# Performance work log

Measured on AMD Instinct MI355X. Metric: run time of the kernel, lower is better.

Reference implementation:

```python
import jax, jax.numpy as jnp
import numpy as np

B, S, D = 1, 2048, 2048
H, G = 32, 8            # n_heads, n_groups
HPG = H // G            # heads per group = 4
HD = D // H             # head_dim = 64


def setup_inputs() -> dict:
    key = jax.random.key(0)
    ks = jax.random.split(key, 5)
    w_scale = 0.02
    return {
        "x":  jax.random.normal(ks[0], (B, S, D), dtype=jnp.float32),
        "Wq": jax.random.normal(ks[1], (D, D), dtype=jnp.float32) * w_scale,
        "bq": jnp.zeros((D,), dtype=jnp.float32),
        "Wk": jax.random.normal(ks[2], (G * HD, D), dtype=jnp.float32) * w_scale,
        "bk": jnp.zeros((G * HD,), dtype=jnp.float32),
        "Wv": jax.random.normal(ks[3], (G * HD, D), dtype=jnp.float32) * w_scale,
        "bv": jnp.zeros((G * HD,), dtype=jnp.float32),
        "Wo": jax.random.normal(ks[4], (D, D), dtype=jnp.float32) * w_scale,
        "bo": jnp.zeros((D,), dtype=jnp.float32),
    }


def reference(x, Wq, bq, Wk, bk, Wv, bv, Wo, bo):
    b, n, _ = x.shape
    # projections (torch Linear: y = x @ W.T + b)
    q = x @ Wq.T + bq                              # [b, n, D]
    k = x @ Wk.T + bk                              # [b, n, G*HD]
    v = x @ Wv.T + bv                              # [b, n, G*HD]
    # q: [b, n, H, HD] -> [b, H, n, HD] -> split heads as (g h): [b, G, HPG, n, HD]
    q = q.reshape(b, n, H, HD).transpose(0, 2, 1, 3).reshape(b, G, HPG, n, HD)
    k = k.reshape(b, n, G, HD).transpose(0, 2, 1, 3)   # [b, G, n, HD]
    v = v.reshape(b, n, G, HD).transpose(0, 2, 1, 3)   # [b, G, n, HD]
    scale = 1.0 / jnp.sqrt(jnp.asarray(HD, dtype=q.dtype))
    attn_score = jnp.einsum('bghnd,bgsd->bghns', q, k) * scale
    attn_prob = jax.nn.softmax(attn_score, axis=-1)
    out = jnp.einsum('bghns,bgsd->bghnd', attn_prob, v)   # [b, G, HPG, n, HD]
    # faithful to original: rearrange 'b g h n d -> b n (h g d)' (h-major, g-minor)
    out = out.transpose(0, 3, 2, 1, 4).reshape(b, n, HPG * G * HD)
    return out @ Wo.T + bo
```

## Files before the change

### kernel.cpp

```cpp
#include <hip/hip_runtime.h>
#include <hip/hip_bf16.h>

constexpr int kS   = 2048;
constexpr int kD   = 2048;
constexpr int kG   = 8;
constexpr int kHD  = 64;
constexpr int kGHD = 512;
constexpr int kNQKV = kD + 2 * kGHD;

constexpr float kQScale = 0.125f * 1.4426950408889634f;

typedef __attribute__((ext_vector_type(8)))  _Float16 f16x8;
typedef __attribute__((ext_vector_type(4)))  float    f32x4;
typedef __attribute__((ext_vector_type(16))) float    f32x16;
typedef __attribute__((ext_vector_type(4)))  unsigned int u32x4;

__device__ __forceinline__ ushort f2h(float x) {
    return __builtin_bit_cast(ushort, (_Float16)x);
}
__device__ __forceinline__ float fast_exp2(float x) {
    return __builtin_amdgcn_exp2f(x);
}
__device__ __forceinline__ unsigned int pkrtz(float a, float b) {
    auto r = __builtin_amdgcn_cvt_pkrtz(a, b);
    return __builtin_bit_cast(unsigned int, r);
}

__global__ __launch_bounds__(256) void cvt_f16(
    const float* __restrict__ in, ushort* __restrict__ out, int n, float scale)
{
    const int i = (blockIdx.x * 256 + threadIdx.x) * 4;
    if (i >= n) return;
    const float4 x = *(const float4*)&in[i];
    ushort4 o;
    o.x = f2h(x.x * scale); o.y = f2h(x.y * scale);
    o.z = f2h(x.z * scale); o.w = f2h(x.w * scale);
    *(ushort4*)&out[i] = o;
}

__global__ __launch_bounds__(256) void prep_bias(
    const float* __restrict__ bq, const float* __restrict__ bk,
    const float* __restrict__ bv, float* __restrict__ bqkv)
{
    const int i = blockIdx.x * 256 + threadIdx.x;
    if (i < kD)             bqkv[i] = bq[i] * kQScale;
    else if (i < kD + kGHD) bqkv[i] = bk[i - kD];
    else if (i < kNQKV)     bqkv[i] = bv[i - kD - kGHD];
}

__device__ __forceinline__ int xcd_swizzle(int orig, int nwg) {
    const int cpx = nwg >> 3;
    return (orig & 7) * cpx + (orig >> 3);
}

#define GEMM_PRELUDE(Aptr, Bptr)                                              \
    const int bid  = xcd_swizzle(blockIdx.x, gridDim.x);                      \
    const int m0   = (bid / gridX) * 128;                                     \
    const int n0   = (bid % gridX) * 128;                                     \
    const int tid  = threadIdx.x;                                             \
    const int w    = tid >> 6;                                                \
    const int lane = tid & 63;                                                \
    const int wm   = w >> 2;                                                  \
    const int wn   = w & 3;                                                   \
    const int fr   = lane & 15;                                               \
    const int kq   = lane >> 4;                                               \
    const int srow = w * 16 + (lane >> 2);                                    \
    const int sslot = ((lane & 3) ^ ((lane >> 3) & 3)) * 8;                   \
    const ushort* gA = (Aptr) + (size_t)(m0 + srow) * K + sslot;              \
    const ushort* gB = (Bptr) + (size_t)(n0 + srow) * K + sslot;              \
    const int pslot = (kq ^ ((fr >> 1) & 3)) * 8;                             \
    f32x4 acc[4][2];                                                          \
    _Pragma("unroll")                                                         \
    for (int mi = 0; mi < 4; ++mi)                                            \
        _Pragma("unroll")                                                     \
        for (int ni = 0; ni < 2; ++ni) {                                      \
            f32x4 z = {0.f, 0.f, 0.f, 0.f};                                   \
            acc[mi][ni] = z;                                                  \
        }

#define GEMM_STAGE(buf, k0)                                                   \
    do {                                                                      \
        __builtin_amdgcn_global_load_lds(                                     \
            (const __attribute__((address_space(1))) void*)(gA + (k0)),       \
            (__attribute__((address_space(3))) void*)&lds[buf][0][w * 512],   \
            16, 0, 0);                                                        \
        __builtin_amdgcn_global_load_lds(                                     \
            (const __attribute__((address_space(1))) void*)(gB + (k0)),       \
            (__attribute__((address_space(3))) void*)&lds[buf][1][w * 512],   \
            16, 0, 0);                                                        \
    } while (0)

#define GEMM_KLOOP(MFMA_BODY)                                                 \
    GEMM_STAGE(0, 0);                                                         \
    __syncthreads();                                                          \
    int cur = 0;                                                              \
    for (int k0 = 0; k0 < K; k0 += 32) {                                      \
        if (k0 + 32 < K) GEMM_STAGE(cur ^ 1, k0 + 32);                        \
        f16x8 af[4], bf[2];                                                   \
        _Pragma("unroll")                                                     \
        for (int f = 0; f < 4; ++f)                                           \
            af[f] = *(const f16x8*)&lds[cur][0][(wm * 64 + f * 16 + fr) * 32 + pslot]; \
        _Pragma("unroll")                                                     \
        for (int f = 0; f < 2; ++f)                                           \
            bf[f] = *(const f16x8*)&lds[cur][1][(wn * 32 + f * 16 + fr) * 32 + pslot]; \
        __builtin_amdgcn_s_setprio(1);                                        \
        MFMA_BODY                                                             \
        __builtin_amdgcn_s_setprio(0);                                        \
        __syncthreads();                                                      \
        cur ^= 1;                                                             \
    }

__global__ __launch_bounds__(512) void gemm_qkv(
    const ushort* __restrict__ Af, const ushort* __restrict__ Bf,
    const float* __restrict__ bias,
    ushort* __restrict__ qb16, ushort* __restrict__ kb16, ushort* __restrict__ vt16,
    int K, int gridX)
{
    __shared__ ushort lds[2][2][128 * 32];

    GEMM_PRELUDE(Af, Bf)
    GEMM_KLOOP(
        _Pragma("unroll")
        for (int mi = 0; mi < 4; ++mi)
            _Pragma("unroll")
            for (int ni = 0; ni < 2; ++ni)
                acc[mi][ni] = __builtin_amdgcn_mfma_f32_16x16x32_f16(
                    af[mi], bf[ni], acc[mi][ni], 0, 0, 0);
    )

    const int seg = (n0 < kD) ? 0 : (n0 < kD + kGHD) ? 1 : 2;
    #pragma unroll
    for (int ni = 0; ni < 2; ++ni) {
        const int ncol = n0 + wn * 32 + ni * 16 + fr;
        const float bv = bias[ncol];
        #pragma unroll
        for (int mi = 0; mi < 4; ++mi) {
            #pragma unroll
            for (int i = 0; i < 4; ++i) {
                const int row = m0 + wm * 64 + mi * 16 + kq * 4 + i;
                const ushort u = f2h(acc[mi][ni][i] + bv);
                if (seg == 0)      qb16[(size_t)row * kD   + ncol]              = u;
                else if (seg == 1) kb16[(size_t)row * kGHD + (ncol - kD)]       = u;
                else               vt16[(size_t)(ncol - kD - kGHD) * kS + row]  = u;
            }
        }
    }
}

__global__ __launch_bounds__(512) void gemm_o(
    const ushort* __restrict__ Af, const ushort* __restrict__ Bf,
    const float* __restrict__ bias, float* __restrict__ C, int K, int N, int gridX)
{
    __shared__ ushort lds[2][2][128 * 32];

    GEMM_PRELUDE(Af, Bf)
    GEMM_KLOOP(
        _Pragma("unroll")
        for (int mi = 0; mi < 4; ++mi)
            _Pragma("unroll")
            for (int ni = 0; ni < 2; ++ni)
                acc[mi][ni] = __builtin_amdgcn_mfma_f32_16x16x32_f16(
                    af[mi], bf[ni], acc[mi][ni], 0, 0, 0);
    )

    #pragma unroll
    for (int ni = 0; ni < 2; ++ni) {
        const int ncol = n0 + wn * 32 + ni * 16 + fr;
        const float bv = bias[ncol];
        #pragma unroll
        for (int mi = 0; mi < 4; ++mi)
            #pragma unroll
            for (int i = 0; i < 4; ++i) {
                const int row = m0 + wm * 64 + mi * 16 + kq * 4 + i;
                C[(size_t)row * N + ncol] = acc[mi][ni][i] + bv;
            }
    }
}

__global__ __launch_bounds__(512) void gqa_attn_mfma(
    const ushort* __restrict__ qb,
    const ushort* __restrict__ kb,
    const ushort* __restrict__ vt,
    ushort* __restrict__ oh)
{
    __shared__ ushort Kt[2][2][64 * 64];
    __shared__ ushort Vt[2][2][64 * 64];

    const int g    = blockIdx.y;
    const int q0   = blockIdx.x * 32;
    const int tid  = threadIdx.x;
    const int w    = tid >> 6;
    const int lane = tid & 63;
    const int hw   = w & 3;
    const int half = w >> 2;
    const int ql   = lane & 31;
    const int hi   = lane >> 5;
    const int h    = g * 4 + hw;
    const int tbase = half * (kS / 2);

    const int r0 = hw * 16 + (lane >> 3);
    const int ss = (lane & 7) ^ (r0 & 7);

#define ATTN_STAGE(buf, t)                                                         \
    do {                                                                           \
        __builtin_amdgcn_global_load_lds(                                          \
            (const __attribute__((address_space(1))) void*)                       \
                (kb + (size_t)(tbase + (t) + r0) * kGHD + g * kHD + ss * 8),       \
            (__attribute__((address_space(3))) void*)(&Kt[half][buf][(hw * 16) * 64]), \
            16, 0, 0);                                                             \
        __builtin_amdgcn_global_load_lds(                                          \
            (const __attribute__((address_space(1))) void*)                       \
                (kb + (size_t)(tbase + (t) + r0 + 8) * kGHD + g * kHD + ss * 8),   \
            (__attribute__((address_space(3))) void*)(&Kt[half][buf][(hw * 16 + 8) * 64]), \
            16, 0, 0);                                                             \
        __builtin_amdgcn_global_load_lds(                                          \
            (const __attribute__((address_space(1))) void*)                       \
                (vt + (size_t)(g * kHD + r0) * kS + tbase + (t) + ss * 8),         \
            (__attribute__((address_space(3))) void*)(&Vt[half][buf][(hw * 16) * 64]), \
            16, 0, 0);                                                             \
        __builtin_amdgcn_global_load_lds(                                          \
            (const __attribute__((address_space(1))) void*)                       \
                (vt + (size_t)(g * kHD + r0 + 8) * kS + tbase + (t) + ss * 8),     \
            (__attribute__((address_space(3))) void*)(&Vt[half][buf][(hw * 16 + 8) * 64]), \
            16, 0, 0);                                                             \
    } while (0)

    ATTN_STAGE(0, 0);

    f16x8 qf[4];
    #pragma unroll
    for (int ks = 0; ks < 4; ++ks)
        qf[ks] = *(const f16x8*)&qb[(size_t)(q0 + ql) * kD + h * kHD + ks * 16 + hi * 8];

    float mrow = -1e30f, lrow = 0.f;
    f32x16 oacc[2];
    #pragma unroll
    for (int db = 0; db < 2; ++db)
        #pragma unroll
        for (int r = 0; r < 16; ++r) oacc[db][r] = 0.f;

    int cur = 0;
    for (int t = 0; t < kS / 2; t += 64) {
        __syncthreads();

        if (t + 64 < kS / 2) ATTN_STAGE(cur ^ 1, t + 64);

        f32x16 sc[2];
        #pragma unroll
        for (int kb2 = 0; kb2 < 2; ++kb2)
            #pragma unroll
            for (int r = 0; r < 16; ++r) sc[kb2][r] = 0.f;

        #pragma unroll
        for (int kb2 = 0; kb2 < 2; ++kb2) {
            #pragma unroll
            for (int ks = 0; ks < 4; ++ks) {
                const f16x8 kf = *(const f16x8*)&Kt[half][cur][(kb2 * 32 + ql) * 64
                                     + (((2 * ks + hi) ^ (ql & 7)) * 8)];
                __builtin_amdgcn_s_setprio(1);
                sc[kb2] = __builtin_amdgcn_mfma_f32_32x32x16_f16(
                    kf, qf[ks], sc[kb2], 0, 0, 0);
                __builtin_amdgcn_s_setprio(0);
            }
        }

        float mt = sc[0][0];
        #pragma unroll
        for (int kb2 = 0; kb2 < 2; ++kb2)
            #pragma unroll
            for (int r = 0; r < 16; ++r) mt = fmaxf(mt, sc[kb2][r]);
        mt = fmaxf(mt, __shfl_xor(mt, 32));

        if (__any(mt > mrow + 11.5f)) {
            const float mnew = (mt > mrow + 11.5f) ? mt : mrow;
            const float c = fast_exp2(mrow - mnew);
            lrow *= c;
            mrow = mnew;
            #pragma unroll
            for (int db = 0; db < 2; ++db)
                #pragma unroll
                for (int r = 0; r < 16; ++r) oacc[db][r] *= c;
        }

        float ps = 0.f;
        #pragma unroll
        for (int kb2 = 0; kb2 < 2; ++kb2)
            #pragma unroll
            for (int r = 0; r < 16; ++r) {
                const float p = fast_exp2(sc[kb2][r] - mrow);
                sc[kb2][r] = p;
                ps += p;
            }
        ps += __shfl_xor(ps, 32);
        lrow += ps;

        #pragma unroll
        for (int kb2 = 0; kb2 < 2; ++kb2) {
            #pragma unroll
            for (int ks = 0; ks < 2; ++ks) {
                unsigned int a0 = pkrtz(sc[kb2][8 * ks + 0], sc[kb2][8 * ks + 1]);
                unsigned int a1 = pkrtz(sc[kb2][8 * ks + 2], sc[kb2][8 * ks + 3]);
                unsigned int b0 = pkrtz(sc[kb2][8 * ks + 4], sc[kb2][8 * ks + 5]);
                unsigned int b1 = pkrtz(sc[kb2][8 * ks + 6], sc[kb2][8 * ks + 7]);
                asm volatile("v_permlane32_swap_b32 %0, %1"
                             : "+v"(a0), "+v"(b0));
                asm volatile("v_permlane32_swap_b32 %0, %1"
                             : "+v"(a1), "+v"(b1));
                const u32x4 pu = {a0, a1, b0, b1};
                const f16x8 pf = __builtin_bit_cast(f16x8, pu);
                #pragma unroll
                for (int db = 0; db < 2; ++db) {
                    const f16x8 vf = *(const f16x8*)&Vt[half][cur][(db * 32 + ql) * 64
                                         + (((4 * kb2 + 2 * ks + hi) ^ (ql & 7)) * 8)];
                    __builtin_amdgcn_s_setprio(1);
                    oacc[db] = __builtin_amdgcn_mfma_f32_32x32x16_f16(
                        vf, pf, oacc[db], 0, 0, 0);
                    __builtin_amdgcn_s_setprio(0);
                }
            }
        }
        cur ^= 1;
    }
#undef ATTN_STAGE

    __syncthreads();
    float* ox  = (float*)(&Kt[0][0][0]);
    float* mlx = (float*)(&Vt[0][0][0]);
    const int idx = hw * 64 + lane;

    if (half == 1) {
        #pragma unroll
        for (int db = 0; db < 2; ++db)
            #pragma unroll
            for (int r = 0; r < 16; ++r)
                ox[(db * 16 + r) * 256 + idx] = oacc[db][r];
        mlx[idx]       = mrow;
        mlx[256 + idx] = lrow;
    }
    __syncthreads();

    if (half == 0) {
        const float m2 = mlx[idx];
        const float l2 = mlx[256 + idx];
        const float mm = fmaxf(mrow, m2);
        const float c1 = fast_exp2(mrow - mm);
        const float c2 = fast_exp2(m2 - mm);
        const float inv = 1.f / (lrow * c1 + l2 * c2);
        const size_t rowbase = (size_t)(q0 + ql) * kD + hw * kGHD + g * kHD;
        #pragma unroll
        for (int db = 0; db < 2; ++db) {
            #pragma unroll
            for (int rr = 0; rr < 4; ++rr) {
                ushort4 o4;
                o4.x = f2h((oacc[db][rr * 4 + 0] * c1 + ox[(db * 16 + rr * 4 + 0) * 256 + idx] * c2) * inv);
                o4.y = f2h((oacc[db][rr * 4 + 1] * c1 + ox[(db * 16 + rr * 4 + 1) * 256 + idx] * c2) * inv);
                o4.z = f2h((oacc[db][rr * 4 + 2] * c1 + ox[(db * 16 + rr * 4 + 2) * 256 + idx] * c2) * inv);
                o4.w = f2h((oacc[db][rr * 4 + 3] * c1 + ox[(db * 16 + rr * 4 + 3) * 256 + idx] * c2) * inv);
                *(ushort4*)&oh[rowbase + db * 32 + rr * 8 + hi * 4] = o4;
            }
        }
    }
}

extern "C" void kernel_launch(void* const* d_in, const int* in_sizes, int n_in,
                              void* d_out, int out_size, void* d_ws, size_t ws_size,
                              hipStream_t stream)
{
    const float* x  = (const float*)d_in[0];
    const float* Wq = (const float*)d_in[1];
    const float* bq = (const float*)d_in[2];
    const float* Wk = (const float*)d_in[3];
    const float* bk = (const float*)d_in[4];
    const float* Wv = (const float*)d_in[5];
    const float* bv = (const float*)d_in[6];
    const float* Wo = (const float*)d_in[7];
    const float* bo = (const float*)d_in[8];
    float* out = (float*)d_out;

    char* p = (char*)d_ws;
    ushort* xf    = (ushort*)p; p += (size_t)kS * kD * 2;
    ushort* wqkvf = (ushort*)p; p += (size_t)kNQKV * kD * 2;
    ushort* wof   = (ushort*)p; p += (size_t)kD * kD * 2;
    float*  bqkv  = (float*)p;  p += 16384;
    ushort* qb16  = (ushort*)p; p += (size_t)kS * kD * 2;
    ushort* kb16  = (ushort*)p; p += (size_t)kS * kGHD * 2;
    ushort* vt16  = (ushort*)p; p += (size_t)kGHD * kS * 2;
    ushort* aoh   = (ushort*)p;

    cvt_f16<<<kS * kD / 1024, 256, 0, stream>>>(x, xf, kS * kD, 1.f);
    cvt_f16<<<kD * kD / 1024, 256, 0, stream>>>(Wq, wqkvf, kD * kD, kQScale);
    cvt_f16<<<kGHD * kD / 1024, 256, 0, stream>>>(Wk, wqkvf + (size_t)kD * kD, kGHD * kD, 1.f);
    cvt_f16<<<kGHD * kD / 1024, 256, 0, stream>>>(
        Wv, wqkvf + (size_t)(kD + kGHD) * kD, kGHD * kD, 1.f);
    cvt_f16<<<kD * kD / 1024, 256, 0, stream>>>(Wo, wof, kD * kD, 1.f);
    prep_bias<<<(kNQKV + 255) / 256, 256, 0, stream>>>(bq, bk, bv, bqkv);

    gemm_qkv<<<(kNQKV / 128) * (kS / 128), 512, 0, stream>>>(
        xf, wqkvf, bqkv, qb16, kb16, vt16, kD, kNQKV / 128);

    gqa_attn_mfma<<<dim3(kS / 32, kG), 512, 0, stream>>>(qb16, kb16, vt16, aoh);

    gemm_o<<<(kD / 128) * (kS / 128), 512, 0, stream>>>(
        aoh, wof, bo, out, kD, kD, kD / 128);
}
```

Measured before the change: 149.0 us.

## Fuse conversion kernels into one launch and batch LDS loads before MFMAs

Replaces the five fp32-to-fp16 conversion launches and the bias prep launch with a single kernel that picks its source and destination by flat index, cutting launch overhead. In the attention kernel, all K and V fragments for a tile are loaded from LDS before the MFMA chains, and setprio is raised once around each chain so the matrix ops issue back to back. It also sets a minimum-occupancy hint on the attention kernel. Holding the hoisted fragments costs more registers, which may conflict with the occupancy hint and cause spills.

```diff
diff --git a/kernel.cpp b/kernel.cpp
--- a/kernel.cpp
+++ b/kernel.cpp
@@ -26,26 +26,43 @@
     return __builtin_bit_cast(unsigned int, r);
 }
 
-__global__ __launch_bounds__(256) void cvt_f16(
-    const float* __restrict__ in, ushort* __restrict__ out, int n, float scale)
+__global__ __launch_bounds__(256) void cvt_all(
+    const float* __restrict__ x,  const float* __restrict__ Wq,
+    const float* __restrict__ Wk, const float* __restrict__ Wv,
+    const float* __restrict__ Wo, const float* __restrict__ bq,
+    const float* __restrict__ bk, const float* __restrict__ bv,
+    ushort* __restrict__ xf, ushort* __restrict__ wqkvf,
+    ushort* __restrict__ wof, float* __restrict__ bqkv)
 {
-    const int i = (blockIdx.x * 256 + threadIdx.x) * 4;
-    if (i >= n) return;
-    const float4 x = *(const float4*)&in[i];
+    constexpr size_t Nx  = (size_t)kS * kD;
+    constexpr size_t NWq = (size_t)kD * kD;
+    constexpr size_t NWk = (size_t)kGHD * kD;
+    constexpr size_t e1 = Nx, e2 = e1 + NWq, e3 = e2 + NWk, e4 = e3 + NWk,
+                     e5 = e4 + NWq;
+    const size_t i = ((size_t)blockIdx.x * 256 + threadIdx.x) * 4;
+
+    const float* src; ushort* dst; float scale = 1.f;
+    if (i < e1)      { src = x  + i;        dst = xf + i; }
+    else if (i < e2) { src = Wq + (i - e1); dst = wqkvf + (i - e1); scale = kQScale; }
+    else if (i < e3) { src = Wk + (i - e2); dst = wqkvf + NWq + (i - e2); }
+    else if (i < e4) { src = Wv + (i - e3); dst = wqkvf + NWq + NWk + (i - e3); }
+    else if (i < e5) { src = Wo + (i - e4); dst = wof + (i - e4); }
+    else {
+        const size_t j = i - e5;
+        #pragma unroll
+        for (int u = 0; u < 4; ++u) {
+            const size_t jj = j + u;
+            if (jj < kD)              bqkv[jj] = bq[jj] * kQScale;
+            else if (jj < kD + kGHD)  bqkv[jj] = bk[jj - kD];
+            else if (jj < (size_t)kNQKV) bqkv[jj] = bv[jj - kD - kGHD];
+        }
+        return;
+    }
+    const float4 v = *(const float4*)src;
     ushort4 o;
-    o.x = f2h(x.x * scale); o.y = f2h(x.y * scale);
-    o.z = f2h(x.z * scale); o.w = f2h(x.w * scale);
-    *(ushort4*)&out[i] = o;
-}
-
-__global__ __launch_bounds__(256) void prep_bias(
-    const float* __restrict__ bq, const float* __restrict__ bk,
-    const float* __restrict__ bv, float* __restrict__ bqkv)
-{
-    const int i = blockIdx.x * 256 + threadIdx.x;
-    if (i < kD)             bqkv[i] = bq[i] * kQScale;
-    else if (i < kD + kGHD) bqkv[i] = bk[i - kD];
-    else if (i < kNQKV)     bqkv[i] = bv[i - kD - kGHD];
+    o.x = f2h(v.x * scale); o.y = f2h(v.y * scale);
+    o.z = f2h(v.z * scale); o.w = f2h(v.w * scale);
+    *(ushort4*)dst = o;
 }
 
 __device__ __forceinline__ int xcd_swizzle(int orig, int nwg) {
@@ -177,7 +194,7 @@
     }
 }
 
-__global__ __launch_bounds__(512) void gqa_attn_mfma(
+__global__ __launch_bounds__(512, 4) void gqa_attn_mfma(
     const ushort* __restrict__ qb,
     const ushort* __restrict__ kb,
     const ushort* __restrict__ vt,
@@ -251,17 +268,21 @@
             #pragma unroll
             for (int r = 0; r < 16; ++r) sc[kb2][r] = 0.f;
 
-        #pragma unroll
-        for (int kb2 = 0; kb2 < 2; ++kb2) {
+        {
+            f16x8 kf[2][4];
+            #pragma unroll
+            for (int kb2 = 0; kb2 < 2; ++kb2)
+                #pragma unroll
+                for (int ks = 0; ks < 4; ++ks)
+                    kf[kb2][ks] = *(const f16x8*)&Kt[half][cur][(kb2 * 32 + ql) * 64
+                                       + (((2 * ks + hi) ^ (ql & 7)) * 8)];
+            __builtin_amdgcn_s_setprio(1);
             #pragma unroll
             for (int ks = 0; ks < 4; ++ks) {
-                const f16x8 kf = *(const f16x8*)&Kt[half][cur][(kb2 * 32 + ql) * 64
-                                     + (((2 * ks + hi) ^ (ql & 7)) * 8)];
-                __builtin_amdgcn_s_setprio(1);
-                sc[kb2] = __builtin_amdgcn_mfma_f32_32x32x16_f16(
-                    kf, qf[ks], sc[kb2], 0, 0, 0);
-                __builtin_amdgcn_s_setprio(0);
+                sc[0] = __builtin_amdgcn_mfma_f32_32x32x16_f16(kf[0][ks], qf[ks], sc[0], 0, 0, 0);
+                sc[1] = __builtin_amdgcn_mfma_f32_32x32x16_f16(kf[1][ks], qf[ks], sc[1], 0, 0, 0);
             }
+            __builtin_amdgcn_s_setprio(0);
         }
 
         float mt = sc[0][0];
@@ -294,30 +315,40 @@
         ps += __shfl_xor(ps, 32);
         lrow += ps;
 
-        #pragma unroll
-        for (int kb2 = 0; kb2 < 2; ++kb2) {
-            #pragma unroll
-            for (int ks = 0; ks < 2; ++ks) {
-                unsigned int a0 = pkrtz(sc[kb2][8 * ks + 0], sc[kb2][8 * ks + 1]);
-                unsigned int a1 = pkrtz(sc[kb2][8 * ks + 2], sc[kb2][8 * ks + 3]);
-                unsigned int b0 = pkrtz(sc[kb2][8 * ks + 4], sc[kb2][8 * ks + 5]);
-                unsigned int b1 = pkrtz(sc[kb2][8 * ks + 6], sc[kb2][8 * ks + 7]);
-                asm volatile("v_permlane32_swap_b32 %0, %1"
-                             : "+v"(a0), "+v"(b0));
-                asm volatile("v_permlane32_swap_b32 %0, %1"
-                             : "+v"(a1), "+v"(b1));
-                const u32x4 pu = {a0, a1, b0, b1};
-                const f16x8 pf = __builtin_bit_cast(f16x8, pu);
+        {
+            f16x8 pf[2][2];
+            #pragma unroll
+            for (int kb2 = 0; kb2 < 2; ++kb2)
                 #pragma unroll
-                for (int db = 0; db < 2; ++db) {
-                    const f16x8 vf = *(const f16x8*)&Vt[half][cur][(db * 32 + ql) * 64
-                                         + (((4 * kb2 + 2 * ks + hi) ^ (ql & 7)) * 8)];
-                    __builtin_amdgcn_s_setprio(1);
-                    oacc[db] = __builtin_amdgcn_mfma_f32_32x32x16_f16(
-                        vf, pf, oacc[db], 0, 0, 0);
-                    __builtin_amdgcn_s_setprio(0);
+                for (int ks = 0; ks < 2; ++ks) {
+                    unsigned int a0 = pkrtz(sc[kb2][8 * ks + 0], sc[kb2][8 * ks + 1]);
+                    unsigned int a1 = pkrtz(sc[kb2][8 * ks + 2], sc[kb2][8 * ks + 3]);
+                    unsigned int b0 = pkrtz(sc[kb2][8 * ks + 4], sc[kb2][8 * ks + 5]);
+                    unsigned int b1 = pkrtz(sc[kb2][8 * ks + 6], sc[kb2][8 * ks + 7]);
+                    asm volatile("v_permlane32_swap_b32 %0, %1" : "+v"(a0), "+v"(b0));
+                    asm volatile("v_permlane32_swap_b32 %0, %1" : "+v"(a1), "+v"(b1));
+                    const u32x4 pu = {a0, a1, b0, b1};
+                    pf[kb2][ks] = __builtin_bit_cast(f16x8, pu);
                 }
-            }
+            f16x8 vf[2][2][2];
+            #pragma unroll
+            for (int kb2 = 0; kb2 < 2; ++kb2)
+                #pragma unroll
+                for (int ks = 0; ks < 2; ++ks)
+                    #pragma unroll
+                    for (int db = 0; db < 2; ++db)
+                        vf[kb2][ks][db] = *(const f16x8*)&Vt[half][cur][(db * 32 + ql) * 64
+                                             + (((4 * kb2 + 2 * ks + hi) ^ (ql & 7)) * 8)];
+            __builtin_amdgcn_s_setprio(1);
+            #pragma unroll
+            for (int kb2 = 0; kb2 < 2; ++kb2)
+                #pragma unroll
+                for (int ks = 0; ks < 2; ++ks)
+                    #pragma unroll
+                    for (int db = 0; db < 2; ++db)
+                        oacc[db] = __builtin_amdgcn_mfma_f32_32x32x16_f16(
+                            vf[kb2][ks][db], pf[kb2][ks], oacc[db], 0, 0, 0);
+            __builtin_amdgcn_s_setprio(0);
         }
         cur ^= 1;
     }
@@ -387,13 +418,10 @@
     ushort* vt16  = (ushort*)p; p += (size_t)kGHD * kS * 2;
     ushort* aoh   = (ushort*)p;
 
-    cvt_f16<<<kS * kD / 1024, 256, 0, stream>>>(x, xf, kS * kD, 1.f);
-    cvt_f16<<<kD * kD / 1024, 256, 0, stream>>>(Wq, wqkvf, kD * kD, kQScale);
-    cvt_f16<<<kGHD * kD / 1024, 256, 0, stream>>>(Wk, wqkvf + (size_t)kD * kD, kGHD * kD, 1.f);
-    cvt_f16<<<kGHD * kD / 1024, 256, 0, stream>>>(
-        Wv, wqkvf + (size_t)(kD + kGHD) * kD, kGHD * kD, 1.f);
-    cvt_f16<<<kD * kD / 1024, 256, 0, stream>>>(Wo, wof, kD * kD, 1.f);
-    prep_bias<<<(kNQKV + 255) / 256, 256, 0, stream>>>(bq, bk, bv, bqkv);
+    constexpr size_t kCvtElems = (size_t)kS * kD + 2 * (size_t)kD * kD
+                               + 2 * (size_t)kGHD * kD + kNQKV;
+    cvt_all<<<(kCvtElems + 1023) / 1024, 256, 0, stream>>>(
+        x, Wq, Wk, Wv, Wo, bq, bk, bv, xf, wqkvf, wof, bqkv);
 
     gemm_qkv<<<(kNQKV / 128) * (kS / 128), 512, 0, stream>>>(
         xf, wqkvf, bqkv, qb16, kb16, vt16, kD, kNQKV / 128);
```

After: 141.0 us. -5.4%, faster.
